# Kernel tuning notes

Hardware: AMD Instinct MI355X
Metric: run time of the kernel (lower is better)

## Reference

```python
import jax, jax.numpy as jnp
import numpy as np

N_NODES = 100000
D_FEAT = 128
N_EDGES = 600000


def setup_inputs() -> dict:
    key = jax.random.key(0)
    k_h, k_s, k_d = jax.random.split(key, 3)
    h = jax.random.normal(k_h, (N_NODES, D_FEAT), dtype=jnp.float32)
    src = jax.random.randint(k_s, (N_EDGES,), 0, N_NODES, dtype=jnp.int64)
    dst = jax.random.randint(k_d, (N_EDGES,), 0, N_NODES, dtype=jnp.int64)
    return {"h": h, "src": src, "dst": dst}


def reference(h, src, dst):
    # u_dot_v: per-edge dot product of gathered node features -> [E, 1]
    score = jnp.sum(h[src] * h[dst], axis=-1, keepdims=True)
    # min/max computed on detached scores in the original (numpy detach)
    mn = jax.lax.stop_gradient(jnp.min(score))
    mx = jax.lax.stop_gradient(jnp.max(score))
    norm = (score - mn) / (mx - mn)
    # python loop in original: 0 stays 0, anything else -> 1 (binary threshold)
    out = jnp.where(norm == 0, jnp.zeros_like(norm), jnp.ones_like(norm))
    return out
```

## Files before the change

kernel.cpp:

```cpp
#include <hip/hip_runtime.h>
#include <float.h>


#define MARGIN 4.0f

__device__ __forceinline__ unsigned enc_key(float f) {
    unsigned u = __float_as_uint(f);
    return (u & 0x80000000u) ? ~u : (u | 0x80000000u);
}
__device__ __forceinline__ float dec_key(unsigned k) {
    unsigned u = (k & 0x80000000u) ? (k ^ 0x80000000u) : ~k;
    return __uint_as_float(u);
}
__device__ __forceinline__ float b2f(unsigned short s) {
    return __uint_as_float(((unsigned)s) << 16);
}
__device__ __forceinline__ unsigned short f2b(float f) {
    unsigned u = __float_as_uint(f);
    unsigned r = 0x7FFFu + ((u >> 16) & 1u);
    return (unsigned short)((u + r) >> 16);
}

__global__ void __launch_bounds__(256) convert_kernel(
    const float4* __restrict__ in, ushort4* __restrict__ outv, int n4) {
    const int stride = gridDim.x * blockDim.x;
    for (int i = blockIdx.x * blockDim.x + threadIdx.x; i < n4; i += stride) {
        float4 f = in[i];
        ushort4 u;
        u.x = f2b(f.x); u.y = f2b(f.y); u.z = f2b(f.z); u.w = f2b(f.w);
        outv[i] = u;
    }
}

__global__ void __launch_bounds__(256) edge_dot_bf16_kernel(
    const ushort* __restrict__ hb,
    const int* __restrict__ src,
    const int* __restrict__ dst,
    float* __restrict__ score,
    unsigned int* __restrict__ keys,
    int nEdges) {
    const int tid  = threadIdx.x;
    const int lane = tid & 63;
    const int half = lane >> 5;
    const int l32  = lane & 31;
    const int wid  = blockIdx.x * (blockDim.x >> 6) + (tid >> 6);
    const int nW   = gridDim.x * (blockDim.x >> 6);

    const ushort4* hb4 = reinterpret_cast<const ushort4*>(hb);

    float localMin = FLT_MAX;
    const int nG = nEdges >> 4;
    for (int g = wid; g < nG; g += nW) {
        const int e = g << 4;
        const int4 s0 = *reinterpret_cast<const int4*>(src + e);
        const int4 s1 = *reinterpret_cast<const int4*>(src + e + 4);
        const int4 s2 = *reinterpret_cast<const int4*>(src + e + 8);
        const int4 s3 = *reinterpret_cast<const int4*>(src + e + 12);
        const int4 d0 = *reinterpret_cast<const int4*>(dst + e);
        const int4 d1 = *reinterpret_cast<const int4*>(dst + e + 4);
        const int4 d2 = *reinterpret_cast<const int4*>(dst + e + 8);
        const int4 d3 = *reinterpret_cast<const int4*>(dst + e + 12);
        const int si[16] = {s0.x,s0.y,s0.z,s0.w, s1.x,s1.y,s1.z,s1.w,
                            s2.x,s2.y,s2.z,s2.w, s3.x,s3.y,s3.z,s3.w};
        const int di[16] = {d0.x,d0.y,d0.z,d0.w, d1.x,d1.y,d1.z,d1.w,
                            d2.x,d2.y,d2.z,d2.w, d3.x,d3.y,d3.z,d3.w};

        ushort4 A[8], B[8];
        #pragma unroll
        for (int p = 0; p < 8; ++p) {
            const int es = half ? si[2*p+1] : si[2*p];
            const int ed = half ? di[2*p+1] : di[2*p];
            A[p] = hb4[es * 32 + l32];
            B[p] = hb4[ed * 32 + l32];
        }

        #pragma unroll
        for (int p = 0; p < 8; ++p) {
            float v = fmaf(b2f(A[p].x), b2f(B[p].x),
                      fmaf(b2f(A[p].y), b2f(B[p].y),
                      fmaf(b2f(A[p].z), b2f(B[p].z),
                           b2f(A[p].w) * b2f(B[p].w))));
            #pragma unroll
            for (int off = 16; off > 0; off >>= 1)
                v += __shfl_xor(v, off, 64);
            if (l32 == 0) score[e + 2*p + half] = v;
            localMin = fminf(localMin, v);
        }
    }

    for (int e = (nG << 4) + wid; e < nEdges; e += nW) {
        const int s = src[e];
        const int d = dst[e];
        const ushort2 a = *reinterpret_cast<const ushort2*>(hb + (size_t)s * 128 + lane * 2);
        const ushort2 b = *reinterpret_cast<const ushort2*>(hb + (size_t)d * 128 + lane * 2);
        float v = fmaf(b2f(a.x), b2f(b.x), b2f(a.y) * b2f(b.y));
        #pragma unroll
        for (int off = 32; off > 0; off >>= 1)
            v += __shfl_xor(v, off, 64);
        if (lane == 0) score[e] = v;
        localMin = fminf(localMin, v);
    }

    #pragma unroll
    for (int off = 32; off > 0; off >>= 1)
        localMin = fminf(localMin, __shfl_xor(localMin, off, 64));
    __shared__ float red[4];
    if (lane == 0) red[tid >> 6] = localMin;
    __syncthreads();
    if (tid == 0) {
        float m = fminf(fminf(red[0], red[1]), fminf(red[2], red[3]));
        atomicMin(keys, enc_key(m));
    }
}

__global__ void __launch_bounds__(256) refine_kernel(
    const float* __restrict__ h,
    const int* __restrict__ src,
    const int* __restrict__ dst,
    float* __restrict__ score,
    unsigned int* __restrict__ keys,
    int nEdges) {
    const float thresh = dec_key(keys[0]) + MARGIN;
    const int stride = gridDim.x * blockDim.x;
    for (int e = blockIdx.x * blockDim.x + threadIdx.x; e < nEdges; e += stride) {
        float s = score[e];
        if (s <= thresh) {
            const float* ra = h + (size_t)src[e] * 128;
            const float* rb = h + (size_t)dst[e] * 128;
            float acc = 0.0f;
            #pragma unroll 4
            for (int i = 0; i < 128; ++i) acc = fmaf(ra[i], rb[i], acc);
            score[e] = acc;
            atomicMin(keys + 1, enc_key(acc));
        }
    }
}

__global__ void __launch_bounds__(256) threshold_kernel(
    float4* __restrict__ out,
    const unsigned int* __restrict__ keys,
    int n4) {
    const float emin = dec_key(keys[1]);
    const int stride = gridDim.x * blockDim.x;
    for (int i = blockIdx.x * blockDim.x + threadIdx.x; i < n4; i += stride) {
        float4 v = out[i];
        v.x = (v.x == emin) ? 0.0f : 1.0f;
        v.y = (v.y == emin) ? 0.0f : 1.0f;
        v.z = (v.z == emin) ? 0.0f : 1.0f;
        v.w = (v.w == emin) ? 0.0f : 1.0f;
        out[i] = v;
    }
}

__global__ void __launch_bounds__(256) edge_dot_f32_kernel(
    const float* __restrict__ h,
    const int* __restrict__ src,
    const int* __restrict__ dst,
    float* __restrict__ score,
    unsigned int* __restrict__ keys,
    int nEdges) {
    const int lane = threadIdx.x & 63;
    const int wid  = blockIdx.x * (blockDim.x >> 6) + (threadIdx.x >> 6);
    const int nW   = gridDim.x * (blockDim.x >> 6);
    float localMin = FLT_MAX;
    const int nG = nEdges >> 3;
    for (int g = wid; g < nG; g += nW) {
        const int e = g << 3;
        const int4 s0 = *reinterpret_cast<const int4*>(src + e);
        const int4 s1 = *reinterpret_cast<const int4*>(src + e + 4);
        const int4 d0 = *reinterpret_cast<const int4*>(dst + e);
        const int4 d1 = *reinterpret_cast<const int4*>(dst + e + 4);
        const int si[8] = {s0.x,s0.y,s0.z,s0.w,s1.x,s1.y,s1.z,s1.w};
        const int di[8] = {d0.x,d0.y,d0.z,d0.w,d1.x,d1.y,d1.z,d1.w};
        float2 a[8], b[8];
        #pragma unroll
        for (int k = 0; k < 8; ++k) {
            a[k] = *reinterpret_cast<const float2*>(h + (size_t)si[k] * 128 + lane * 2);
            b[k] = *reinterpret_cast<const float2*>(h + (size_t)di[k] * 128 + lane * 2);
        }
        #pragma unroll
        for (int k = 0; k < 8; ++k) {
            float v = fmaf(a[k].y, b[k].y, a[k].x * b[k].x);
            #pragma unroll
            for (int off = 32; off > 0; off >>= 1) v += __shfl_xor(v, off, 64);
            if (lane == 0) score[e + k] = v;
            localMin = fminf(localMin, v);
        }
    }
    for (int e = (nG << 3) + wid; e < nEdges; e += nW) {
        const float2 a = *reinterpret_cast<const float2*>(h + (size_t)src[e] * 128 + lane * 2);
        const float2 b = *reinterpret_cast<const float2*>(h + (size_t)dst[e] * 128 + lane * 2);
        float v = fmaf(a.y, b.y, a.x * b.x);
        #pragma unroll
        for (int off = 32; off > 0; off >>= 1) v += __shfl_xor(v, off, 64);
        if (lane == 0) score[e] = v;
        localMin = fminf(localMin, v);
    }
    if (lane == 0) atomicMin(keys + 1, enc_key(localMin));
}

extern "C" void kernel_launch(void* const* d_in, const int* in_sizes, int n_in,
                              void* d_out, int out_size, void* d_ws, size_t ws_size,
                              hipStream_t stream) {
    const float* h  = (const float*)d_in[0];
    const int* src  = (const int*)d_in[1];
    const int* dst  = (const int*)d_in[2];
    float* out      = (float*)d_out;
    unsigned* keys  = (unsigned*)d_ws;
    const int nH     = in_sizes[0];
    const int nEdges = in_sizes[1];
    const int n4     = nEdges >> 2;

    hipMemsetAsync(d_ws, 0xFF, 8, stream);

    const size_t need = 256 + (size_t)nH * 2;
    if (ws_size >= need && (nEdges & 3) == 0) {
        ushort* hb = (ushort*)((char*)d_ws + 256);
        convert_kernel<<<2048, 256, 0, stream>>>(
            (const float4*)h, (ushort4*)hb, nH >> 2);
        edge_dot_bf16_kernel<<<2048, 256, 0, stream>>>(
            hb, src, dst, out, keys, nEdges);
        refine_kernel<<<1024, 256, 0, stream>>>(h, src, dst, out, keys, nEdges);
    } else {
        edge_dot_f32_kernel<<<2048, 256, 0, stream>>>(h, src, dst, out, keys, nEdges);
    }

    int blocks = (n4 + 255) / 256;
    if (blocks > 2048) blocks = 2048;
    threshold_kernel<<<blocks, 256, 0, stream>>>(
        reinterpret_cast<float4*>(out), keys, n4);
}
```

Before: 151.8 us.

## Store node features as fp8 e5m2 and compute edge dots with half2 FMAs

The node feature copy is quantized to 8-bit e5m2 instead of bf16, which halves the bytes gathered per edge. Each edge is now handled by 8 lanes with 16-byte loads, and the dot product uses packed half2 FMAs. The refine margin grows from 4 to 12 to absorb the larger quantization error, which likely sends more edges to the exact fp32 refine pass. Accuracy depends on that margin: fp16 accumulation could overflow or lose precision.

```diff
diff --git a/kernel.cpp b/kernel.cpp
--- a/kernel.cpp
+++ b/kernel.cpp
@@ -1,8 +1,9 @@
 #include <hip/hip_runtime.h>
+#include <hip/hip_fp16.h>
 #include <float.h>
 
 
-#define MARGIN 4.0f
+#define MARGIN 12.0f
 
 __device__ __forceinline__ unsigned enc_key(float f) {
     unsigned u = __float_as_uint(f);
@@ -12,28 +13,42 @@
     unsigned u = (k & 0x80000000u) ? (k ^ 0x80000000u) : ~k;
     return __uint_as_float(u);
 }
-__device__ __forceinline__ float b2f(unsigned short s) {
-    return __uint_as_float(((unsigned)s) << 16);
-}
-__device__ __forceinline__ unsigned short f2b(float f) {
-    unsigned u = __float_as_uint(f);
-    unsigned r = 0x7FFFu + ((u >> 16) & 1u);
-    return (unsigned short)((u + r) >> 16);
+__device__ __forceinline__ unsigned f2e5m2(float f) {
+    unsigned short hb = __builtin_bit_cast(unsigned short, __float2half(f));
+    unsigned r = 0x7Fu + ((hb >> 8) & 1u);
+    return (((unsigned)hb + r) >> 8) & 0xFFu;
+}
+__device__ __forceinline__ __half2 h2lo(unsigned u) {
+    return __builtin_bit_cast(__half2, __builtin_amdgcn_perm(u, 0u, 0x050C040Cu));
+}
+__device__ __forceinline__ __half2 h2hi(unsigned u) {
+    return __builtin_bit_cast(__half2, __builtin_amdgcn_perm(u, 0u, 0x070C060Cu));
+}
+__device__ __forceinline__ float dot16(uint4 A, uint4 B) {
+    __half2 acc = __builtin_bit_cast(__half2, 0u);
+    acc = __hfma2(h2lo(A.x), h2lo(B.x), acc);
+    acc = __hfma2(h2hi(A.x), h2hi(B.x), acc);
+    acc = __hfma2(h2lo(A.y), h2lo(B.y), acc);
+    acc = __hfma2(h2hi(A.y), h2hi(B.y), acc);
+    acc = __hfma2(h2lo(A.z), h2lo(B.z), acc);
+    acc = __hfma2(h2hi(A.z), h2hi(B.z), acc);
+    acc = __hfma2(h2lo(A.w), h2lo(B.w), acc);
+    acc = __hfma2(h2hi(A.w), h2hi(B.w), acc);
+    return __low2float(acc) + __high2float(acc);
 }
 
 __global__ void __launch_bounds__(256) convert_kernel(
-    const float4* __restrict__ in, ushort4* __restrict__ outv, int n4) {
+    const float4* __restrict__ in, unsigned* __restrict__ outb, int n4) {
     const int stride = gridDim.x * blockDim.x;
     for (int i = blockIdx.x * blockDim.x + threadIdx.x; i < n4; i += stride) {
         float4 f = in[i];
-        ushort4 u;
-        u.x = f2b(f.x); u.y = f2b(f.y); u.z = f2b(f.z); u.w = f2b(f.w);
-        outv[i] = u;
-    }
-}
-
-__global__ void __launch_bounds__(256) edge_dot_bf16_kernel(
-    const ushort* __restrict__ hb,
+        outb[i] = f2e5m2(f.x) | (f2e5m2(f.y) << 8) |
+                  (f2e5m2(f.z) << 16) | (f2e5m2(f.w) << 24);
+    }
+}
+
+__global__ void __launch_bounds__(256) edge_dot_fp8_kernel(
+    const uint4* __restrict__ hb4,
     const int* __restrict__ src,
     const int* __restrict__ dst,
     float* __restrict__ score,
@@ -41,62 +56,44 @@
     int nEdges) {
     const int tid  = threadIdx.x;
     const int lane = tid & 63;
-    const int half = lane >> 5;
-    const int l32  = lane & 31;
+    const int oct  = lane >> 3;
+    const int l8   = lane & 7;
     const int wid  = blockIdx.x * (blockDim.x >> 6) + (tid >> 6);
     const int nW   = gridDim.x * (blockDim.x >> 6);
-
-    const ushort4* hb4 = reinterpret_cast<const ushort4*>(hb);
 
     float localMin = FLT_MAX;
     const int nG = nEdges >> 4;
     for (int g = wid; g < nG; g += nW) {
         const int e = g << 4;
-        const int4 s0 = *reinterpret_cast<const int4*>(src + e);
-        const int4 s1 = *reinterpret_cast<const int4*>(src + e + 4);
-        const int4 s2 = *reinterpret_cast<const int4*>(src + e + 8);
-        const int4 s3 = *reinterpret_cast<const int4*>(src + e + 12);
-        const int4 d0 = *reinterpret_cast<const int4*>(dst + e);
-        const int4 d1 = *reinterpret_cast<const int4*>(dst + e + 4);
-        const int4 d2 = *reinterpret_cast<const int4*>(dst + e + 8);
-        const int4 d3 = *reinterpret_cast<const int4*>(dst + e + 12);
-        const int si[16] = {s0.x,s0.y,s0.z,s0.w, s1.x,s1.y,s1.z,s1.w,
-                            s2.x,s2.y,s2.z,s2.w, s3.x,s3.y,s3.z,s3.w};
-        const int di[16] = {d0.x,d0.y,d0.z,d0.w, d1.x,d1.y,d1.z,d1.w,
-                            d2.x,d2.y,d2.z,d2.w, d3.x,d3.y,d3.z,d3.w};
-
-        ushort4 A[8], B[8];
-        #pragma unroll
-        for (int p = 0; p < 8; ++p) {
-            const int es = half ? si[2*p+1] : si[2*p];
-            const int ed = half ? di[2*p+1] : di[2*p];
-            A[p] = hb4[es * 32 + l32];
-            B[p] = hb4[ed * 32 + l32];
-        }
-
-        #pragma unroll
-        for (int p = 0; p < 8; ++p) {
-            float v = fmaf(b2f(A[p].x), b2f(B[p].x),
-                      fmaf(b2f(A[p].y), b2f(B[p].y),
-                      fmaf(b2f(A[p].z), b2f(B[p].z),
-                           b2f(A[p].w) * b2f(B[p].w))));
-            #pragma unroll
-            for (int off = 16; off > 0; off >>= 1)
-                v += __shfl_xor(v, off, 64);
-            if (l32 == 0) score[e + 2*p + half] = v;
-            localMin = fminf(localMin, v);
-        }
+        const int sA0 = src[e + oct];
+        const int sA1 = src[e + 8 + oct];
+        const int sB0 = dst[e + oct];
+        const int sB1 = dst[e + 8 + oct];
+        const uint4 A0 = hb4[(size_t)sA0 * 8 + l8];
+        const uint4 A1 = hb4[(size_t)sA1 * 8 + l8];
+        const uint4 B0 = hb4[(size_t)sB0 * 8 + l8];
+        const uint4 B1 = hb4[(size_t)sB1 * 8 + l8];
+
+        float v0 = dot16(A0, B0);
+        float v1 = dot16(A1, B1);
+        #pragma unroll
+        for (int off = 1; off < 8; off <<= 1) {
+            v0 += __shfl_xor(v0, off, 64);
+            v1 += __shfl_xor(v1, off, 64);
+        }
+        if (l8 == 0) {
+            score[e + oct]     = v0;
+            score[e + 8 + oct] = v1;
+        }
+        localMin = fminf(localMin, fminf(v0, v1));
     }
 
     for (int e = (nG << 4) + wid; e < nEdges; e += nW) {
-        const int s = src[e];
-        const int d = dst[e];
-        const ushort2 a = *reinterpret_cast<const ushort2*>(hb + (size_t)s * 128 + lane * 2);
-        const ushort2 b = *reinterpret_cast<const ushort2*>(hb + (size_t)d * 128 + lane * 2);
-        float v = fmaf(b2f(a.x), b2f(b.x), b2f(a.y) * b2f(b.y));
-        #pragma unroll
-        for (int off = 32; off > 0; off >>= 1)
-            v += __shfl_xor(v, off, 64);
+        const uint4 a = hb4[(size_t)src[e] * 8 + l8];
+        const uint4 b = hb4[(size_t)dst[e] * 8 + l8];
+        float v = dot16(a, b);
+        #pragma unroll
+        for (int off = 1; off < 8; off <<= 1) v += __shfl_xor(v, off, 64);
         if (lane == 0) score[e] = v;
         localMin = fminf(localMin, v);
     }
@@ -213,13 +210,13 @@
 
     hipMemsetAsync(d_ws, 0xFF, 8, stream);
 
-    const size_t need = 256 + (size_t)nH * 2;
-    if (ws_size >= need && (nEdges & 3) == 0) {
-        ushort* hb = (ushort*)((char*)d_ws + 256);
+    const size_t need = 256 + (size_t)nH;
+    if (ws_size >= need && (nEdges & 3) == 0 && (nH & 3) == 0) {
+        unsigned* hb = (unsigned*)((char*)d_ws + 256);
         convert_kernel<<<2048, 256, 0, stream>>>(
-            (const float4*)h, (ushort4*)hb, nH >> 2);
-        edge_dot_bf16_kernel<<<2048, 256, 0, stream>>>(
-            hb, src, dst, out, keys, nEdges);
+            (const float4*)h, hb, nH >> 2);
+        edge_dot_fp8_kernel<<<2048, 256, 0, stream>>>(
+            (const uint4*)hb, src, dst, out, keys, nEdges);
         refine_kernel<<<1024, 256, 0, stream>>>(h, src, dst, out, keys, nEdges);
     } else {
         edge_dot_f32_kernel<<<2048, 256, 0, stream>>>(h, src, dst, out, keys, nEdges);
```

New measurement: 136.3 us. 1.11x faster.
